# Optimization experiments

Measured on AMD Instinct MI355X. Metric: run time of the kernel, lower is better.

Reference implementation:

```python
import jax, jax.numpy as jnp
import numpy as np

N_NODES = 50000
N_EDGES = 800000
D = 128


def setup_inputs() -> dict:
    key = jax.random.key(0)
    ks = jax.random.split(key, 8)
    s = 1.0 / np.sqrt(D)
    return {
        "x": jax.random.normal(ks[0], (N_NODES, D), dtype=jnp.float32),
        "edge_index": jax.random.randint(ks[1], (2, N_EDGES), 0, N_NODES, dtype=jnp.int32),
        "W0l": jax.random.normal(ks[2], (D, D), dtype=jnp.float32) * s,
        "b0l": jnp.zeros((D,), dtype=jnp.float32),
        "W0r": jax.random.normal(ks[3], (D, D), dtype=jnp.float32) * s,
        "W1l": jax.random.normal(ks[4], (D, D), dtype=jnp.float32) * s,
        "b1l": jnp.zeros((D,), dtype=jnp.float32),
        "W1r": jax.random.normal(ks[5], (D, D), dtype=jnp.float32) * s,
    }


def reference(x, edge_index, W0l, b0l, W0r, W1l, b1l, W1r):
    # Encoder(conv='sage', num_layers=2), eval mode (dropout = identity).
    src = edge_index[0]  # x_j gathered from source nodes
    dst = edge_index[1]  # aggregated at target nodes
    # in-degree for mean aggregation; isolated nodes get 0 aggregate (PyG mean)
    deg = jax.ops.segment_sum(jnp.ones_like(dst, dtype=x.dtype), dst, num_segments=N_NODES)
    inv_deg = jnp.where(deg > 0, 1.0 / jnp.maximum(deg, 1.0), 0.0)[:, None]

    def sage(h, Wl, bl, Wr):
        m = h @ Wl + bl                                        # lin_l
        agg = jax.ops.segment_sum(m[src], dst, num_segments=N_NODES) * inv_deg  # mean aggr
        return agg + h @ Wr                                    # + lin_r skip

    h = jax.nn.relu(sage(x, W0l, b0l, W0r))   # layer 0 + relu
    return sage(h, W1l, b1l, W1r)             # final layer
```

## Files before the change

kernel.cpp:

```cpp
#include <hip/hip_runtime.h>

#define N_NODES 50000
#define N_EDGES 800000
#define D 128
#define CAP64 64
#define EIDXN (N_NODES * CAP64)

typedef __bf16 bf16x8 __attribute__((ext_vector_type(8)));
typedef short s16x8 __attribute__((ext_vector_type(8)));
typedef float f32x4 __attribute__((ext_vector_type(4)));
typedef float f32x2 __attribute__((ext_vector_type(2)));
typedef unsigned short u16;
typedef unsigned int u32;
typedef unsigned char u8;
typedef u32 u32x2 __attribute__((ext_vector_type(2)));
typedef u32 u32x4 __attribute__((ext_vector_type(4)));
typedef u16 u16x4 __attribute__((ext_vector_type(4)));

__device__ inline u16 f32_to_bf16(float f) {
    u32 u = __builtin_bit_cast(u32, f);
    u += 0x7fffu + ((u >> 16) & 1u);
    return (u16)(u >> 16);
}

__device__ inline f32x4 mfma16(s16x8 a, s16x8 b, f32x4 c) {
    return __builtin_amdgcn_mfma_f32_16x16x32_bf16(
        __builtin_bit_cast(bf16x8, a), __builtin_bit_cast(bf16x8, b), c, 0, 0, 0);
}

#define CAST_BLOCKS ((N_NODES * 16) / 256)
#define CUR_BLOCKS ((N_NODES + 255) / 256)
#define FILL_BLOCKS ((EIDXN / 2 + 1023) / 1024)

__global__ __launch_bounds__(256) void prep_stage(
    const float* __restrict__ x, u16* __restrict__ xb,
    u8* __restrict__ xf8, u8* __restrict__ hf8,
    const float* __restrict__ W0l, const float* __restrict__ W0r,
    const float* __restrict__ W1l, const float* __restrict__ W1r,
    u16* __restrict__ Wp, int* __restrict__ cursor,
    u16* __restrict__ eidx) {
    int t = threadIdx.x, b = blockIdx.x;
    if (b < CAST_BLOCKS) {
        int gid = b * 256 + t;
        const float* p = x + (size_t)gid * 8;
        f32x4 a = *(const f32x4*)p;
        f32x4 c = *(const f32x4*)(p + 4);
        u16 o[8];
#pragma unroll
        for (int j = 0; j < 4; j++) { o[j] = f32_to_bf16(a[j]); o[4 + j] = f32_to_bf16(c[j]); }
        *(s16x8*)(xb + (size_t)gid * 8) = *(const s16x8*)o;
        int p0 = __builtin_amdgcn_cvt_pk_fp8_f32(a.x, a.y, 0, false);
        int p1 = __builtin_amdgcn_cvt_pk_fp8_f32(a.z, a.w, 0, false);
        int p2 = __builtin_amdgcn_cvt_pk_fp8_f32(c.x, c.y, 0, false);
        int p3 = __builtin_amdgcn_cvt_pk_fp8_f32(c.z, c.w, 0, false);
        u32x2 w;
        w.x = (u32)(p0 & 0xffff) | ((u32)(p1 & 0xffff) << 16);
        w.y = (u32)(p2 & 0xffff) | ((u32)(p3 & 0xffff) << 16);
        *(u32x2*)(xf8 + (size_t)gid * 8) = w;
    } else if (b < CAST_BLOCKS + 32) {
        int gid = (b - CAST_BLOCKS) * 256 + t;
        int wsel = gid >> 11;
        int rem  = gid & 2047;
        int ct   = rem >> 8;
        int ks   = (rem >> 6) & 3;
        int lane = rem & 63;
        const float* W = (wsel == 0) ? W0l : (wsel == 1) ? W0r : (wsel == 2) ? W1l : W1r;
        int n  = ct * 16 + (lane & 15);
        int k0 = ks * 32 + (lane >> 4) * 8;
        u16 o[8];
#pragma unroll
        for (int j = 0; j < 8; j++) o[j] = f32_to_bf16(W[(k0 + j) * D + n]);
        u16* dp = Wp + wsel * 16384 + (size_t)((ct * 4 + ks) * 64 + lane) * 8;
        *(s16x8*)dp = *(const s16x8*)o;
    } else if (b < CAST_BLOCKS + 33) {
        if (t < 32)       ((u32*)(xf8 + (size_t)N_NODES * D))[t] = 0;
        else if (t < 64)  ((u32*)(hf8 + (size_t)N_NODES * D))[t - 32] = 0;
    } else if (b < CAST_BLOCKS + 33 + CUR_BLOCKS) {
        int n = (b - CAST_BLOCKS - 33) * 256 + t;
        if (n < N_NODES) cursor[n] = n << 6;
    } else {
        int fb = b - CAST_BLOCKS - 33 - CUR_BLOCKS;
        u32x4 pat = (u32x4){0xC350C350u, 0xC350C350u, 0xC350C350u, 0xC350C350u};
        *(u32x4*)((u32*)eidx + (size_t)fb * 1024 + t * 4) = pat;
    }
}

__global__ __launch_bounds__(256) void scatter_kernel(
    const int* __restrict__ src, const int* __restrict__ dst,
    int* __restrict__ cursor, u16* __restrict__ eidx) {
    int i0 = (blockIdx.x * 256 + threadIdx.x) * 4;
    if (i0 >= N_EDGES) return;
    u32x4 s = *(const u32x4*)(src + i0);
    u32x4 d = *(const u32x4*)(dst + i0);
    int sv[4] = {(int)s.x, (int)s.y, (int)s.z, (int)s.w};
    int dv[4] = {(int)d.x, (int)d.y, (int)d.z, (int)d.w};
#pragma unroll
    for (int j = 0; j < 4; j++) {
        int pos = atomicAdd(&cursor[dv[j]], 1);
        int lim = (dv[j] << 6) + (CAP64 - 1);
        if (pos > lim) pos = lim;
        eidx[pos] = (u16)sv[j];
    }
}

__device__ inline void issue_e(u16x4 (&e)[2], const u16* __restrict__ eidx,
                               const int (&basek)[2], const int (&rnds)[2],
                               int quad, int rr) {
#pragma unroll
    for (int k = 0; k < 2; k++)
        if (rr < rnds[k]) e[k] = *(const u16x4*)(eidx + basek[k] + rr * 16 + quad * 4);
}
__device__ inline void issue_g(u32x2 (&g)[2][4], const u16x4 (&e)[2],
                               const u8* __restrict__ AF8, const int (&rnds)[2],
                               int ql, int rr) {
#pragma unroll
    for (int k = 0; k < 2; k++)
        if (rr < rnds[k]) {
#pragma unroll
            for (int j = 0; j < 4; j++)
                g[k][j] = *(const u32x2*)(AF8 + (size_t)e[k][j] * D + ql * 8);
        }
}
__device__ inline void unpack_acc(f32x2 (&acc)[2][4], const u32x2 (&g)[2][4],
                                  const int (&rnds)[2], int rr) {
#pragma unroll
    for (int k = 0; k < 2; k++)
        if (rr < rnds[k]) {
#pragma unroll
            for (int j = 0; j < 4; j++) {
                u32x2 v = g[k][j];
                acc[k][0] += __builtin_amdgcn_cvt_pk_f32_fp8((int)v.x, false);
                acc[k][1] += __builtin_amdgcn_cvt_pk_f32_fp8((int)v.x, true);
                acc[k][2] += __builtin_amdgcn_cvt_pk_f32_fp8((int)v.y, false);
                acc[k][3] += __builtin_amdgcn_cvt_pk_f32_fp8((int)v.y, true);
            }
        }
}

template <int RELU, int OUTF32>
__global__ __launch_bounds__(512) void fused_layer(
    const u16* __restrict__ A, const u8* __restrict__ AF8,
    const u16* __restrict__ WpR, const u16* __restrict__ WpL,
    const float* __restrict__ bias, const int* __restrict__ cursor,
    const u16* __restrict__ eidx,
    u16* __restrict__ outb, u8* __restrict__ outf8, float* __restrict__ outf) {
    __shared__ char mlds[16 * 256];
    int wave = threadIdx.x >> 6, lane = threadIdx.x & 63;
    int rowbase = blockIdx.x * 16;
    int quad = lane >> 4, ql = lane & 15;

    int basek[2], rnds[2], degk[2];
#pragma unroll
    for (int k = 0; k < 2; k++) {
        int node = rowbase + wave * 2 + k;
        int dd = cursor[node] - (node << 6);
        if (dd > CAP64) dd = CAP64;
        degk[k]  = dd;
        basek[k] = node << 6;
        rnds[k]  = (dd + 15) >> 4;
    }
    int maxr = rnds[0] > rnds[1] ? rnds[0] : rnds[1];

    f32x2 acc[2][4];
#pragma unroll
    for (int k = 0; k < 2; k++)
#pragma unroll
        for (int e = 0; e < 4; e++) acc[k][e] = (f32x2){0.f, 0.f};

    if (maxr > 0) {
        u16x4 eA[2], eB[2];
        u32x2 gA[2][4], gB[2][4];
        issue_e(eA, eidx, basek, rnds, quad, 0);
        issue_g(gA, eA, AF8, rnds, ql, 0);
        if (maxr > 1) issue_e(eB, eidx, basek, rnds, quad, 1);
        int r = 0;
        while (true) {
            if (r + 1 < maxr) issue_g(gB, eB, AF8, rnds, ql, r + 1);
            if (r + 2 < maxr) issue_e(eA, eidx, basek, rnds, quad, r + 2);
            unpack_acc(acc, gA, rnds, r);
            if (++r >= maxr) break;
            if (r + 1 < maxr) issue_g(gA, eA, AF8, rnds, ql, r + 1);
            if (r + 2 < maxr) issue_e(eB, eidx, basek, rnds, quad, r + 2);
            unpack_acc(acc, gB, rnds, r);
            if (++r >= maxr) break;
        }
    }

#pragma unroll
    for (int k = 0; k < 2; k++) {
        float v[8];
#pragma unroll
        for (int e = 0; e < 4; e++) { v[2 * e] = acc[k][e].x; v[2 * e + 1] = acc[k][e].y; }
#pragma unroll
        for (int j = 0; j < 8; j++) {
            v[j] += __shfl_xor(v[j], 16);
            v[j] += __shfl_xor(v[j], 32);
        }
        if (quad == 0) {
            float iv = degk[k] > 0 ? 1.0f / (float)degk[k] : 0.0f;
            u32x4 o;
            o.x = (u32)f32_to_bf16(v[0] * iv) | ((u32)f32_to_bf16(v[1] * iv) << 16);
            o.y = (u32)f32_to_bf16(v[2] * iv) | ((u32)f32_to_bf16(v[3] * iv) << 16);
            o.z = (u32)f32_to_bf16(v[4] * iv) | ((u32)f32_to_bf16(v[5] * iv) << 16);
            o.w = (u32)f32_to_bf16(v[6] * iv) | ((u32)f32_to_bf16(v[7] * iv) << 16);
            int lr = wave * 2 + k;
            *(u32x4*)(mlds + lr * 256 + ((ql ^ lr) & 15) * 16) = o;
        }
    }

    s16x8 bR[4], bL[4];
#pragma unroll
    for (int ks = 0; ks < 4; ks++) {
        size_t off = (size_t)((wave * 4 + ks) * 64 + lane) * 8;
        bR[ks] = *(const s16x8*)(WpR + off);
        bL[ks] = *(const s16x8*)(WpL + off);
    }
    __syncthreads();

    f32x4 acc2 = (f32x4){0.f, 0.f, 0.f, 0.f};
#pragma unroll
    for (int ks = 0; ks < 4; ks++) {
        s16x8 a1 = *(const s16x8*)(A + (size_t)(rowbase + ql) * D + ks * 32 + quad * 8);
        s16x8 a2 = *(const s16x8*)(mlds + ql * 256 + (((ks * 4 + quad) ^ ql) & 15) * 16);
        acc2 = mfma16(a1, bR[ks], acc2);
        acc2 = mfma16(a2, bL[ks], acc2);
    }

    float bv = bias[wave * 16 + ql];

#pragma unroll
    for (int i = 0; i < 4; i++) {
        int row = rowbase + quad * 4 + i;
        int dr = cursor[row] - (row << 6);
        float mask = dr > 0 ? 1.f : 0.f;
        int col = wave * 16 + ql;
        float val = acc2[i] + mask * bv;
        if (RELU) val = val > 0.f ? val : 0.f;
        if (OUTF32) {
            outf[(size_t)row * D + col] = val;
        } else {
            outb[(size_t)row * D + col] = f32_to_bf16(val);
            int pk = __builtin_amdgcn_cvt_pk_fp8_f32(val, val, 0, false);
            outf8[(size_t)row * D + col] = (u8)(pk & 0xff);
        }
    }
}

extern "C" void kernel_launch(void* const* d_in, const int* in_sizes, int n_in,
                              void* d_out, int out_size, void* d_ws, size_t ws_size,
                              hipStream_t stream) {
    const float* x    = (const float*)d_in[0];
    const int*   edge = (const int*)d_in[1];
    const int*   src  = edge;
    const int*   dstn = edge + N_EDGES;
    const float* W0l  = (const float*)d_in[2];
    const float* b0l  = (const float*)d_in[3];
    const float* W0r  = (const float*)d_in[4];
    const float* W1l  = (const float*)d_in[5];
    const float* b1l  = (const float*)d_in[6];
    const float* W1r  = (const float*)d_in[7];
    float* out = (float*)d_out;

    char* p = (char*)d_ws;
    auto alloc = [&](size_t nb) { char* r = p; p += (nb + 255) & ~(size_t)255; return r; };
    int*   cursor = (int*)alloc((size_t)N_NODES * 4);
    u16*   eidx   = (u16*)alloc((size_t)(EIDXN + 4096) * 2);
    u16*   xb     = (u16*)alloc((size_t)N_NODES * D * 2);
    u16*   hb     = (u16*)alloc((size_t)N_NODES * D * 2);
    u8*    xf8    = (u8*)alloc((size_t)(N_NODES + 1) * D);
    u8*    hf8    = (u8*)alloc((size_t)(N_NODES + 1) * D);
    u16*   Wp     = (u16*)alloc((size_t)4 * 16384 * 2);

    prep_stage<<<CAST_BLOCKS + 33 + CUR_BLOCKS + FILL_BLOCKS, 256, 0, stream>>>(
        x, xb, xf8, hf8, W0l, W0r, W1l, W1r, Wp, cursor, eidx);
    scatter_kernel<<<(N_EDGES / 4 + 255) / 256, 256, 0, stream>>>(src, dstn, cursor, eidx);

    int fblocks = N_NODES / 16;
    const u16* WpL0 = Wp;
    const u16* WpR0 = Wp + 16384;
    const u16* WpL1 = Wp + 2 * 16384;
    const u16* WpR1 = Wp + 3 * 16384;
    fused_layer<1, 0><<<fblocks, 512, 0, stream>>>(xb, xf8, WpR0, WpL0, b0l, cursor, eidx, hb, hf8, nullptr);
    fused_layer<0, 1><<<fblocks, 512, 0, stream>>>(hb, hf8, WpR1, WpL1, b1l, cursor, eidx, nullptr, nullptr, out);
}
```

Baseline: 229.5 us.

## Fuse edge scatter into prep kernel and drop eidx sentinel fill

Merges the edge-bucketing scatter into the cast/prep kernel so each cast thread also handles one edge, and replaces the cursor init blocks with a memset to zero. The cursor now holds the per-node count instead of an absolute slot. The full 6.4 MB sentinel fill of the edge-index buckets is removed; the gather instead masks slots past the node degree to the zero row at N_NODES. This saves one kernel launch and a large memory write. In exchange the gather does an extra compare per edge, and there is an added memset launch.

```diff
diff --git a/kernel.cpp b/kernel.cpp
--- a/kernel.cpp
+++ b/kernel.cpp
@@ -29,22 +29,23 @@
 }
 
 #define CAST_BLOCKS ((N_NODES * 16) / 256)
-#define CUR_BLOCKS ((N_NODES + 255) / 256)
-#define FILL_BLOCKS ((EIDXN / 2 + 1023) / 1024)
-
-__global__ __launch_bounds__(256) void prep_stage(
+
+__global__ __launch_bounds__(256) void prep_scatter(
     const float* __restrict__ x, u16* __restrict__ xb,
     u8* __restrict__ xf8, u8* __restrict__ hf8,
     const float* __restrict__ W0l, const float* __restrict__ W0r,
     const float* __restrict__ W1l, const float* __restrict__ W1r,
-    u16* __restrict__ Wp, int* __restrict__ cursor,
-    u16* __restrict__ eidx) {
+    u16* __restrict__ Wp,
+    const int* __restrict__ src, const int* __restrict__ dst,
+    int* __restrict__ cursor, u16* __restrict__ eidx) {
     int t = threadIdx.x, b = blockIdx.x;
     if (b < CAST_BLOCKS) {
         int gid = b * 256 + t;
+        int sv = src[gid], dv = dst[gid];
         const float* p = x + (size_t)gid * 8;
         f32x4 a = *(const f32x4*)p;
         f32x4 c = *(const f32x4*)(p + 4);
+        int pos = atomicAdd(&cursor[dv], 1);
         u16 o[8];
 #pragma unroll
         for (int j = 0; j < 4; j++) { o[j] = f32_to_bf16(a[j]); o[4 + j] = f32_to_bf16(c[j]); }
@@ -57,6 +58,8 @@
         w.x = (u32)(p0 & 0xffff) | ((u32)(p1 & 0xffff) << 16);
         w.y = (u32)(p2 & 0xffff) | ((u32)(p3 & 0xffff) << 16);
         *(u32x2*)(xf8 + (size_t)gid * 8) = w;
+        if (pos > CAP64 - 1) pos = CAP64 - 1;
+        eidx[(dv << 6) + pos] = (u16)sv;
     } else if (b < CAST_BLOCKS + 32) {
         int gid = (b - CAST_BLOCKS) * 256 + t;
         int wsel = gid >> 11;
@@ -72,34 +75,9 @@
         for (int j = 0; j < 8; j++) o[j] = f32_to_bf16(W[(k0 + j) * D + n]);
         u16* dp = Wp + wsel * 16384 + (size_t)((ct * 4 + ks) * 64 + lane) * 8;
         *(s16x8*)dp = *(const s16x8*)o;
-    } else if (b < CAST_BLOCKS + 33) {
+    } else {
         if (t < 32)       ((u32*)(xf8 + (size_t)N_NODES * D))[t] = 0;
         else if (t < 64)  ((u32*)(hf8 + (size_t)N_NODES * D))[t - 32] = 0;
-    } else if (b < CAST_BLOCKS + 33 + CUR_BLOCKS) {
-        int n = (b - CAST_BLOCKS - 33) * 256 + t;
-        if (n < N_NODES) cursor[n] = n << 6;
-    } else {
-        int fb = b - CAST_BLOCKS - 33 - CUR_BLOCKS;
-        u32x4 pat = (u32x4){0xC350C350u, 0xC350C350u, 0xC350C350u, 0xC350C350u};
-        *(u32x4*)((u32*)eidx + (size_t)fb * 1024 + t * 4) = pat;
-    }
-}
-
-__global__ __launch_bounds__(256) void scatter_kernel(
-    const int* __restrict__ src, const int* __restrict__ dst,
-    int* __restrict__ cursor, u16* __restrict__ eidx) {
-    int i0 = (blockIdx.x * 256 + threadIdx.x) * 4;
-    if (i0 >= N_EDGES) return;
-    u32x4 s = *(const u32x4*)(src + i0);
-    u32x4 d = *(const u32x4*)(dst + i0);
-    int sv[4] = {(int)s.x, (int)s.y, (int)s.z, (int)s.w};
-    int dv[4] = {(int)d.x, (int)d.y, (int)d.z, (int)d.w};
-#pragma unroll
-    for (int j = 0; j < 4; j++) {
-        int pos = atomicAdd(&cursor[dv[j]], 1);
-        int lim = (dv[j] << 6) + (CAP64 - 1);
-        if (pos > lim) pos = lim;
-        eidx[pos] = (u16)sv[j];
     }
 }
 
@@ -112,13 +90,16 @@
 }
 __device__ inline void issue_g(u32x2 (&g)[2][4], const u16x4 (&e)[2],
                                const u8* __restrict__ AF8, const int (&rnds)[2],
-                               int ql, int rr) {
+                               const int (&degk)[2], int quad, int ql, int rr) {
 #pragma unroll
     for (int k = 0; k < 2; k++)
         if (rr < rnds[k]) {
-#pragma unroll
-            for (int j = 0; j < 4; j++)
-                g[k][j] = *(const u32x2*)(AF8 + (size_t)e[k][j] * D + ql * 8);
+            int sbase = rr * 16 + quad * 4;
+#pragma unroll
+            for (int j = 0; j < 4; j++) {
+                int idx = (sbase + j < degk[k]) ? (int)e[k][j] : N_NODES;
+                g[k][j] = *(const u32x2*)(AF8 + (size_t)idx * D + ql * 8);
+            }
         }
 }
 __device__ inline void unpack_acc(f32x2 (&acc)[2][4], const u32x2 (&g)[2][4],
@@ -153,7 +134,7 @@
 #pragma unroll
     for (int k = 0; k < 2; k++) {
         int node = rowbase + wave * 2 + k;
-        int dd = cursor[node] - (node << 6);
+        int dd = cursor[node];
         if (dd > CAP64) dd = CAP64;
         degk[k]  = dd;
         basek[k] = node << 6;
@@ -171,15 +152,15 @@
         u16x4 eA[2], eB[2];
         u32x2 gA[2][4], gB[2][4];
         issue_e(eA, eidx, basek, rnds, quad, 0);
-        issue_g(gA, eA, AF8, rnds, ql, 0);
+        issue_g(gA, eA, AF8, rnds, degk, quad, ql, 0);
         if (maxr > 1) issue_e(eB, eidx, basek, rnds, quad, 1);
         int r = 0;
         while (true) {
-            if (r + 1 < maxr) issue_g(gB, eB, AF8, rnds, ql, r + 1);
+            if (r + 1 < maxr) issue_g(gB, eB, AF8, rnds, degk, quad, ql, r + 1);
             if (r + 2 < maxr) issue_e(eA, eidx, basek, rnds, quad, r + 2);
             unpack_acc(acc, gA, rnds, r);
             if (++r >= maxr) break;
-            if (r + 1 < maxr) issue_g(gA, eA, AF8, rnds, ql, r + 1);
+            if (r + 1 < maxr) issue_g(gA, eA, AF8, rnds, degk, quad, ql, r + 1);
             if (r + 2 < maxr) issue_e(eB, eidx, basek, rnds, quad, r + 2);
             unpack_acc(acc, gB, rnds, r);
             if (++r >= maxr) break;
@@ -231,8 +212,7 @@
 #pragma unroll
     for (int i = 0; i < 4; i++) {
         int row = rowbase + quad * 4 + i;
-        int dr = cursor[row] - (row << 6);
-        float mask = dr > 0 ? 1.f : 0.f;
+        float mask = cursor[row] > 0 ? 1.f : 0.f;
         int col = wave * 16 + ql;
         float val = acc2[i] + mask * bv;
         if (RELU) val = val > 0.f ? val : 0.f;
@@ -264,16 +244,17 @@
     char* p = (char*)d_ws;
     auto alloc = [&](size_t nb) { char* r = p; p += (nb + 255) & ~(size_t)255; return r; };
     int*   cursor = (int*)alloc((size_t)N_NODES * 4);
-    u16*   eidx   = (u16*)alloc((size_t)(EIDXN + 4096) * 2);
+    u16*   eidx   = (u16*)alloc((size_t)EIDXN * 2);
     u16*   xb     = (u16*)alloc((size_t)N_NODES * D * 2);
     u16*   hb     = (u16*)alloc((size_t)N_NODES * D * 2);
     u8*    xf8    = (u8*)alloc((size_t)(N_NODES + 1) * D);
     u8*    hf8    = (u8*)alloc((size_t)(N_NODES + 1) * D);
     u16*   Wp     = (u16*)alloc((size_t)4 * 16384 * 2);
 
-    prep_stage<<<CAST_BLOCKS + 33 + CUR_BLOCKS + FILL_BLOCKS, 256, 0, stream>>>(
-        x, xb, xf8, hf8, W0l, W0r, W1l, W1r, Wp, cursor, eidx);
-    scatter_kernel<<<(N_EDGES / 4 + 255) / 256, 256, 0, stream>>>(src, dstn, cursor, eidx);
+    hipMemsetAsync(cursor, 0, (size_t)N_NODES * 4, stream);
+
+    prep_scatter<<<CAST_BLOCKS + 33, 256, 0, stream>>>(
+        x, xb, xf8, hf8, W0l, W0r, W1l, W1r, Wp, src, dstn, cursor, eidx);
 
     int fblocks = N_NODES / 16;
     const u16* WpL0 = Wp;
```

Result: faster. 219.9 us (-4.2%).
